# Performance work log

Hardware: AMD Instinct MI355X
Metric: run time of the kernel (lower is better)

## Reference

```python
import jax, jax.numpy as jnp
import numpy as np

B, T, D = 4, 2048, 1024
H = 16
HD = D // H  # 64


def setup_inputs() -> dict:
    key = jax.random.key(0)
    ks = jax.random.split(key, 7)
    scale = 1.0 / np.sqrt(D)
    x = jax.random.normal(ks[0], (B, T, D), dtype=jnp.float32)
    # per-head projection weights, stacked over heads: [H, D, HD]
    Wq = jax.random.normal(ks[1], (H, D, HD), dtype=jnp.float32) * scale
    Wk = jax.random.normal(ks[2], (H, D, HD), dtype=jnp.float32) * scale
    Wv = jax.random.normal(ks[3], (H, D, HD), dtype=jnp.float32) * scale
    s_raw = jnp.zeros((H,), dtype=jnp.float32)  # learnable ssmax scale per head
    proj_W = jax.random.normal(ks[4], (D, D), dtype=jnp.float32) * scale
    proj_b = jax.random.normal(ks[5], (D,), dtype=jnp.float32) * 0.01
    return {"x": x, "Wq": Wq, "Wk": Wk, "Wv": Wv, "s_raw": s_raw,
            "proj_W": proj_W, "proj_b": proj_b}


def reference(x, Wq, Wk, Wv, s_raw, proj_W, proj_b):
    # per-head q/k/v: [B, H, T, HD]
    q = jnp.einsum('btd,hde->bhte', x, Wq)
    k = jnp.einsum('btd,hde->bhte', x, Wk)
    v = jnp.einsum('btd,hde->bhte', x, Wv)

    # ssmax: q scaled by softplus(s) * log(position index, 1-based)
    logn = jnp.log(jnp.arange(1, T + 1, dtype=x.dtype))  # [T]
    s = jax.nn.softplus(s_raw)  # [H]
    q = q * (s[None, :, None, None] * logn[None, None, :, None])

    scores = jnp.einsum('bhte,bhse->bhts', q, k) * (HD ** -0.5)
    causal = jnp.tril(jnp.ones((T, T), dtype=bool))
    scores = jnp.where(causal[None, None], scores, -jnp.inf)
    w = jax.nn.softmax(scores, axis=-1)

    out = jnp.einsum('bhts,bhse->bhte', w, v)          # [B, H, T, HD]
    out = out.transpose(0, 2, 1, 3).reshape(B, T, D)    # concat heads
    return out @ proj_W.T + proj_b
```

## Files before the change

### kernel.cpp

```cpp
#include <hip/hip_runtime.h>
#include <hip/hip_bf16.h>

#define Bv 4
#define Tv 2048
#define Dv 1024
#define Hv 16
#define HDv 64
#define Mv (Bv*Tv)

typedef __hip_bfloat16 bf16;
typedef short s8v __attribute__((ext_vector_type(8)));
typedef float f4v __attribute__((ext_vector_type(4)));
typedef float f16a __attribute__((ext_vector_type(16)));

__device__ __forceinline__ unsigned short f2us(float x){
    bf16 h = __float2bfloat16(x);
    return *reinterpret_cast<unsigned short*>(&h);
}
__device__ __forceinline__ unsigned int pack2(float a, float b){
    return (unsigned int)f2us(a) | ((unsigned int)f2us(b) << 16);
}
__device__ __forceinline__ void glds16(const unsigned short* g, unsigned short* lds_base){
    __builtin_amdgcn_global_load_lds(
        (const __attribute__((address_space(1))) unsigned int*)g,
        (__attribute__((address_space(3))) unsigned int*)lds_base, 16, 0, 0);
}

__global__ void cvt_kernel(const float* __restrict__ src,
                           unsigned short* __restrict__ dst, int n4) {
    int i = blockIdx.x * 256 + threadIdx.x;
    if (i < n4) {
        float4 f = *(const float4*)(src + (size_t)i * 4);
        ushort4 o;
        o.x = f2us(f.x); o.y = f2us(f.y); o.z = f2us(f.z); o.w = f2us(f.w);
        *(ushort4*)(dst + (size_t)i * 4) = o;
    }
}

__global__ __launch_bounds__(256) void wt_kernel(
    const float* __restrict__ Wq, const float* __restrict__ Wk,
    const float* __restrict__ Wv, unsigned short* __restrict__ Wt)
{
    const int dt  = blockIdx.x;
    const int h   = blockIdx.y;
    const int sel = blockIdx.z;
    const float* W = (sel == 0) ? Wq : ((sel == 1) ? Wk : Wv);
    const float* Wh = W + (size_t)h * Dv * HDv;
    __shared__ float Tf[64][65];
    const int tid = threadIdx.x;
    for (int l = 0; l < 16; ++l) {
        int idx = tid + l * 256;
        int r = idx >> 6, e = idx & 63;
        Tf[r][e] = Wh[(size_t)(dt * 64 + r) * HDv + e];
    }
    __syncthreads();
    unsigned short* out = Wt + ((size_t)sel * Hv + h) * HDv * Dv;
    for (int l = 0; l < 16; ++l) {
        int idx = tid + l * 256;
        int e = idx >> 6, d = idx & 63;
        out[(size_t)e * Dv + dt * 64 + d] = f2us(Tf[d][e]);
    }
}

__global__ __launch_bounds__(256) void qkv_big(
    const unsigned short* __restrict__ xb, const unsigned short* __restrict__ Wc,
    const float* __restrict__ s_raw,
    unsigned short* __restrict__ q, unsigned short* __restrict__ k,
    unsigned short* __restrict__ vT)
{
    const int bm = blockIdx.x;
    const int bn = blockIdx.y;
    const int tid = threadIdx.x;
    const int w = tid >> 6, lane = tid & 63;
    const int n16 = lane & 15, quad = lane >> 4;
    const int wm = w >> 1, wn = w & 1;

    __shared__ __align__(16) unsigned short As[128 * 64];
    __shared__ __align__(16) unsigned short Bs[128 * 64];

    f4v acc[4][4];
    f4v zero = {0.f, 0.f, 0.f, 0.f};
    #pragma unroll
    for (int i = 0; i < 4; ++i)
        #pragma unroll
        for (int j = 0; j < 4; ++j) acc[i][j] = zero;

    const int row0 = bm * 128, col0 = bn * 128;
    const int lr = lane >> 3, lc = (lane & 7) * 8;

    for (int k0 = 0; k0 < Dv; k0 += 64) {
        __syncthreads();
        #pragma unroll
        for (int i = 0; i < 4; ++i) {
            int rb = w * 32 + i * 8;
            glds16(xb + (size_t)(row0 + rb + lr) * Dv + k0 + lc, &As[rb * 64]);
            glds16(Wc + (size_t)(col0 + rb + lr) * Dv + k0 + lc, &Bs[rb * 64]);
        }
        __syncthreads();
        #pragma unroll
        for (int ks = 0; ks < 2; ++ks) {
            s8v bfr[4];
            #pragma unroll
            for (int ni = 0; ni < 4; ++ni)
                bfr[ni] = *(const s8v*)(&Bs[(wn * 64 + ni * 16 + n16) * 64 + ks * 32 + quad * 8]);
            #pragma unroll
            for (int mi = 0; mi < 4; ++mi) {
                s8v afr = *(const s8v*)(&As[(wm * 64 + mi * 16 + n16) * 64 + ks * 32 + quad * 8]);
                #pragma unroll
                for (int ni = 0; ni < 4; ++ni)
                    acc[mi][ni] = __builtin_amdgcn_mfma_f32_16x16x32_bf16(afr, bfr[ni], acc[mi][ni], 0, 0, 0);
            }
        }
    }

    #pragma unroll
    for (int ni = 0; ni < 4; ++ni) {
        int n = col0 + wn * 64 + ni * 16 + n16;
        int sel = n >> 10, h = (n >> 6) & 15, e = n & 63;
        if (sel == 2) {
            #pragma unroll
            for (int mi = 0; mi < 4; ++mi) {
                int row = row0 + wm * 64 + mi * 16 + quad * 4;
                int bb_ = row >> 11, t = row & (Tv - 1);
                ushort4 o4;
                o4.x = f2us(acc[mi][ni][0]); o4.y = f2us(acc[mi][ni][1]);
                o4.z = f2us(acc[mi][ni][2]); o4.w = f2us(acc[mi][ni][3]);
                *(ushort4*)(vT + ((size_t)(bb_ * Hv + h) * HDv + e) * Tv + t) = o4;
            }
        } else {
            unsigned short* out = (sel == 0) ? q : k;
            float sc_h = (sel == 0) ? log1pf(expf(s_raw[h])) * 0.125f : 1.0f;
            #pragma unroll
            for (int mi = 0; mi < 4; ++mi) {
                #pragma unroll
                for (int r = 0; r < 4; ++r) {
                    int row = row0 + wm * 64 + mi * 16 + quad * 4 + r;
                    int bb_ = row >> 11, t = row & (Tv - 1);
                    float rs = (sel == 0) ? sc_h * logf((float)(t + 1)) : 1.0f;
                    out[((size_t)(bb_ * Hv + h) * Tv + t) * HDv + e] = f2us(acc[mi][ni][r] * rs);
                }
            }
        }
    }
}

__global__ __launch_bounds__(256) void attn_mfma(
    const unsigned short* __restrict__ q, const unsigned short* __restrict__ k,
    const unsigned short* __restrict__ vT, unsigned short* __restrict__ attn)
{
    const int qt = (Tv / 128 - 1) - (int)blockIdx.x;
    const int bh = blockIdx.y;
    const int b = bh >> 4, h = bh & 15;
    const int tid = threadIdx.x;
    const int w = tid >> 6, lane = tid & 63;
    const int l31 = lane & 31, hi = lane >> 5;

    __shared__ __align__(16) unsigned short Ks[64][72];
    __shared__ __align__(16) unsigned short VTs[64][72];

    const size_t hb = (size_t)(b * Hv + h) * Tv * HDv;
    const int qstrip = qt * 128 + w * 32;
    const int myq = qstrip + l31;

    s8v qf[4];
    #pragma unroll
    for (int ks = 0; ks < 4; ++ks)
        qf[ks] = *(const s8v*)(q + hb + (size_t)myq * HDv + ks * 16 + hi * 8);

    f16a st0, st1, ot0, ot1;
    #pragma unroll
    for (int i = 0; i < 16; ++i) { ot0[i] = 0.f; ot1[i] = 0.f; }
    float lrun = 0.f;

    const int r_ = tid >> 3, g_ = (tid & 7) * 8;
    const int r2 = (tid + 256) >> 3, g2 = (tid & 7) * 8;

    ulonglong2 kr0, kr1, vr0, vr1;
    kr0 = *(const ulonglong2*)(k + hb + (size_t)r_ * HDv + g_);
    vr0 = *(const ulonglong2*)(vT + hb + (size_t)r_ * Tv + 0 + g_);
    kr1 = *(const ulonglong2*)(k + hb + (size_t)r2 * HDv + g2);
    vr1 = *(const ulonglong2*)(vT + hb + (size_t)r2 * Tv + 0 + g2);

    const int ktmax = 2 * qt + 1;
    for (int kt = 0; kt <= ktmax; ++kt) {
        const int s0 = kt * 64;
        __syncthreads();
        *(ulonglong2*)(&Ks[r_][g_]) = kr0;
        *(ulonglong2*)(&VTs[r_][g_]) = vr0;
        *(ulonglong2*)(&Ks[r2][g2]) = kr1;
        *(ulonglong2*)(&VTs[r2][g2]) = vr1;
        __syncthreads();
        if (kt < ktmax) {
            const int sn = s0 + 64;
            kr0 = *(const ulonglong2*)(k + hb + (size_t)(sn + r_) * HDv + g_);
            vr0 = *(const ulonglong2*)(vT + hb + (size_t)r_ * Tv + sn + g_);
            kr1 = *(const ulonglong2*)(k + hb + (size_t)(sn + r2) * HDv + g2);
            vr1 = *(const ulonglong2*)(vT + hb + (size_t)r2 * Tv + sn + g2);
        }
        if (s0 > qstrip + 31) continue;

        #pragma unroll
        for (int i = 0; i < 16; ++i) { st0[i] = 0.f; st1[i] = 0.f; }
        #pragma unroll
        for (int ks = 0; ks < 4; ++ks) {
            s8v a0 = *(const s8v*)(&Ks[l31][ks * 16 + hi * 8]);
            s8v a1 = *(const s8v*)(&Ks[32 + l31][ks * 16 + hi * 8]);
            st0 = __builtin_amdgcn_mfma_f32_32x32x16_bf16(a0, qf[ks], st0, 0, 0, 0);
            st1 = __builtin_amdgcn_mfma_f32_32x32x16_bf16(a1, qf[ks], st1, 0, 0, 0);
        }
        if (s0 + 63 > qstrip) {
            #pragma unroll
            for (int reg = 0; reg < 16; ++reg) {
                int srow = (reg & 3) + 8 * (reg >> 2) + 4 * hi;
                if (s0 + srow > myq)      st0[reg] = -1e30f;
                if (s0 + 32 + srow > myq) st1[reg] = -1e30f;
            }
        }
        float lsum = 0.f;
        #pragma unroll
        for (int i = 0; i < 16; ++i) {
            st0[i] = __expf(st0[i]);
            st1[i] = __expf(st1[i]);
            lsum += st0[i] + st1[i];
        }
        lrun += lsum;

        unsigned int pk[16];
        #pragma unroll
        for (int g = 0; g < 4; ++g) {
            pk[2 * g]         = pack2(st0[4 * g],     st0[4 * g + 1]);
            pk[2 * g + 1]     = pack2(st0[4 * g + 2], st0[4 * g + 3]);
            pk[8 + 2 * g]     = pack2(st1[4 * g],     st1[4 * g + 1]);
            pk[8 + 2 * g + 1] = pack2(st1[4 * g + 2], st1[4 * g + 3]);
        }
        #pragma unroll
        for (int ks = 0; ks < 4; ++ks) {
            int base = (ks >> 1) * 8 + (ks & 1) * 4;
            unsigned int v0 = hi ? pk[base]     : pk[base + 2];
            unsigned int v1 = hi ? pk[base + 1] : pk[base + 3];
            unsigned int r0 = (unsigned int)__shfl_xor((int)v0, 32);
            unsigned int r1 = (unsigned int)__shfl_xor((int)v1, 32);
            union { s8v v; unsigned int d[4]; } bf;
            bf.d[0] = hi ? r0 : pk[base];
            bf.d[1] = hi ? r1 : pk[base + 1];
            bf.d[2] = hi ? pk[base + 2] : r0;
            bf.d[3] = hi ? pk[base + 3] : r1;
            s8v a0 = *(const s8v*)(&VTs[l31][ks * 16 + hi * 8]);
            s8v a1 = *(const s8v*)(&VTs[32 + l31][ks * 16 + hi * 8]);
            ot0 = __builtin_amdgcn_mfma_f32_32x32x16_bf16(a0, bf.v, ot0, 0, 0, 0);
            ot1 = __builtin_amdgcn_mfma_f32_32x32x16_bf16(a1, bf.v, ot1, 0, 0, 0);
        }
    }

    float ltot = lrun + __shfl_xor(lrun, 32);
    float inv = 1.0f / ltot;
    size_t obase = ((size_t)(b * Tv) + myq) * Dv + h * HDv;
    #pragma unroll
    for (int g = 0; g < 4; ++g) {
        ushort4 o4;
        o4.x = f2us(ot0[4 * g]     * inv); o4.y = f2us(ot0[4 * g + 1] * inv);
        o4.z = f2us(ot0[4 * g + 2] * inv); o4.w = f2us(ot0[4 * g + 3] * inv);
        *(ushort4*)(attn + obase + 8 * g + 4 * hi) = o4;
        o4.x = f2us(ot1[4 * g]     * inv); o4.y = f2us(ot1[4 * g + 1] * inv);
        o4.z = f2us(ot1[4 * g + 2] * inv); o4.w = f2us(ot1[4 * g + 3] * inv);
        *(ushort4*)(attn + obase + 32 + 8 * g + 4 * hi) = o4;
    }
}

__global__ __launch_bounds__(256) void proj_big(
    const unsigned short* __restrict__ attn, const unsigned short* __restrict__ Wb,
    const float* __restrict__ bias, float* __restrict__ out)
{
    const int bm = blockIdx.x;
    const int bn = blockIdx.y;
    const int tid = threadIdx.x;
    const int w = tid >> 6, lane = tid & 63;
    const int n16 = lane & 15, quad = lane >> 4;
    const int wm = w >> 1, wn = w & 1;

    __shared__ __align__(16) unsigned short As[128 * 64];
    __shared__ __align__(16) unsigned short Bs[128 * 64];

    f4v acc[4][4];
    f4v zero = {0.f, 0.f, 0.f, 0.f};
    #pragma unroll
    for (int i = 0; i < 4; ++i)
        #pragma unroll
        for (int j = 0; j < 4; ++j) acc[i][j] = zero;

    const int row0 = bm * 128, col0 = bn * 128;
    const int lr = lane >> 3, lc = (lane & 7) * 8;

    for (int k0 = 0; k0 < Dv; k0 += 64) {
        __syncthreads();
        #pragma unroll
        for (int i = 0; i < 4; ++i) {
            int rb = w * 32 + i * 8;
            glds16(attn + (size_t)(row0 + rb + lr) * Dv + k0 + lc, &As[rb * 64]);
            glds16(Wb   + (size_t)(col0 + rb + lr) * Dv + k0 + lc, &Bs[rb * 64]);
        }
        __syncthreads();
        #pragma unroll
        for (int ks = 0; ks < 2; ++ks) {
            s8v bfr[4];
            #pragma unroll
            for (int ni = 0; ni < 4; ++ni)
                bfr[ni] = *(const s8v*)(&Bs[(wn * 64 + ni * 16 + n16) * 64 + ks * 32 + quad * 8]);
            #pragma unroll
            for (int mi = 0; mi < 4; ++mi) {
                s8v afr = *(const s8v*)(&As[(wm * 64 + mi * 16 + n16) * 64 + ks * 32 + quad * 8]);
                #pragma unroll
                for (int ni = 0; ni < 4; ++ni)
                    acc[mi][ni] = __builtin_amdgcn_mfma_f32_16x16x32_bf16(afr, bfr[ni], acc[mi][ni], 0, 0, 0);
            }
        }
    }
    #pragma unroll
    for (int ni = 0; ni < 4; ++ni) {
        int n = col0 + wn * 64 + ni * 16 + n16;
        float bn_ = bias[n];
        #pragma unroll
        for (int mi = 0; mi < 4; ++mi) {
            #pragma unroll
            for (int r = 0; r < 4; ++r) {
                int m = row0 + wm * 64 + mi * 16 + quad * 4 + r;
                out[(size_t)m * Dv + n] = acc[mi][ni][r] + bn_;
            }
        }
    }
}

extern "C" void kernel_launch(void* const* d_in, const int* in_sizes, int n_in,
                              void* d_out, int out_size, void* d_ws, size_t ws_size,
                              hipStream_t stream) {
    const float* x     = (const float*)d_in[0];
    const float* Wq    = (const float*)d_in[1];
    const float* Wk    = (const float*)d_in[2];
    const float* Wv    = (const float*)d_in[3];
    const float* s_raw = (const float*)d_in[4];
    const float* projW = (const float*)d_in[5];
    const float* projb = (const float*)d_in[6];
    float* out = (float*)d_out;

    const size_t nx  = (size_t)Mv * Dv;
    const size_t nqk = (size_t)Bv * Hv * Tv * HDv;
    unsigned short* x_bf = (unsigned short*)d_ws;
    unsigned short* qb   = x_bf + nx;
    unsigned short* kb   = qb + nqk;
    unsigned short* vTb  = kb + nqk;
    unsigned short* Wt   = vTb + nqk;
    unsigned short* Wpb  = Wt + (size_t)3 * Hv * HDv * Dv;
    unsigned short* attn = x_bf;

    cvt_kernel<<<(int)(nx / 4 / 256), 256, 0, stream>>>(x, x_bf, (int)(nx / 4));
    cvt_kernel<<<(int)((size_t)Dv * Dv / 4 / 256), 256, 0, stream>>>(projW, Wpb, Dv * Dv / 4);
    wt_kernel<<<dim3(16, 16, 3), 256, 0, stream>>>(Wq, Wk, Wv, Wt);
    qkv_big<<<dim3(Mv / 128, 3072 / 128), 256, 0, stream>>>(x_bf, Wt, s_raw, qb, kb, vTb);
    attn_mfma<<<dim3(Tv / 128, Bv * Hv), 256, 0, stream>>>(qb, kb, vTb, attn);
    proj_big<<<dim3(Mv / 128, Dv / 128), 256, 0, stream>>>(attn, Wpb, projb, out);
}
```

Baseline: 326.5 us.

## Load K/V MFMA operands directly from global memory, dropping LDS staging

The attention kernel no longer stages K and V^T tiles through shared memory with block-wide barriers and register prefetch. Each wave now loads its MFMA operand fragments straight from global memory and runs only up to its own causal limit, with no __syncthreads. This removes barrier and LDS traffic and lets each wave stop at its own diagonal, but the four waves of a block now each fetch the same K/V data through cache and lose the software prefetch, so load latency is exposed.

```diff
diff --git a/kernel.cpp b/kernel.cpp
--- a/kernel.cpp
+++ b/kernel.cpp
@@ -155,10 +155,9 @@
     const int w = tid >> 6, lane = tid & 63;
     const int l31 = lane & 31, hi = lane >> 5;
 
-    __shared__ __align__(16) unsigned short Ks[64][72];
-    __shared__ __align__(16) unsigned short VTs[64][72];
-
     const size_t hb = (size_t)(b * Hv + h) * Tv * HDv;
+    const unsigned short* kb = k + hb;
+    const unsigned short* vb = vT + hb;
     const int qstrip = qt * 128 + w * 32;
     const int myq = qstrip + l31;
 
@@ -172,41 +171,29 @@
     for (int i = 0; i < 16; ++i) { ot0[i] = 0.f; ot1[i] = 0.f; }
     float lrun = 0.f;
 
-    const int r_ = tid >> 3, g_ = (tid & 7) * 8;
-    const int r2 = (tid + 256) >> 3, g2 = (tid & 7) * 8;
-
-    ulonglong2 kr0, kr1, vr0, vr1;
-    kr0 = *(const ulonglong2*)(k + hb + (size_t)r_ * HDv + g_);
-    vr0 = *(const ulonglong2*)(vT + hb + (size_t)r_ * Tv + 0 + g_);
-    kr1 = *(const ulonglong2*)(k + hb + (size_t)r2 * HDv + g2);
-    vr1 = *(const ulonglong2*)(vT + hb + (size_t)r2 * Tv + 0 + g2);
-
-    const int ktmax = 2 * qt + 1;
+    const int ktmax = (qstrip + 31) >> 6;
     for (int kt = 0; kt <= ktmax; ++kt) {
         const int s0 = kt * 64;
-        __syncthreads();
-        *(ulonglong2*)(&Ks[r_][g_]) = kr0;
-        *(ulonglong2*)(&VTs[r_][g_]) = vr0;
-        *(ulonglong2*)(&Ks[r2][g2]) = kr1;
-        *(ulonglong2*)(&VTs[r2][g2]) = vr1;
-        __syncthreads();
-        if (kt < ktmax) {
-            const int sn = s0 + 64;
-            kr0 = *(const ulonglong2*)(k + hb + (size_t)(sn + r_) * HDv + g_);
-            vr0 = *(const ulonglong2*)(vT + hb + (size_t)r_ * Tv + sn + g_);
-            kr1 = *(const ulonglong2*)(k + hb + (size_t)(sn + r2) * HDv + g2);
-            vr1 = *(const ulonglong2*)(vT + hb + (size_t)r2 * Tv + sn + g2);
-        }
-        if (s0 > qstrip + 31) continue;
+
+        s8v ka0[4], ka1[4];
+        #pragma unroll
+        for (int ks = 0; ks < 4; ++ks) {
+            ka0[ks] = *(const s8v*)(kb + (size_t)(s0 + l31) * HDv + ks * 16 + hi * 8);
+            ka1[ks] = *(const s8v*)(kb + (size_t)(s0 + 32 + l31) * HDv + ks * 16 + hi * 8);
+        }
+        s8v va0[4], va1[4];
+        #pragma unroll
+        for (int ks = 0; ks < 4; ++ks) {
+            va0[ks] = *(const s8v*)(vb + (size_t)l31 * Tv + s0 + ks * 16 + hi * 8);
+            va1[ks] = *(const s8v*)(vb + (size_t)(32 + l31) * Tv + s0 + ks * 16 + hi * 8);
+        }
 
         #pragma unroll
         for (int i = 0; i < 16; ++i) { st0[i] = 0.f; st1[i] = 0.f; }
         #pragma unroll
         for (int ks = 0; ks < 4; ++ks) {
-            s8v a0 = *(const s8v*)(&Ks[l31][ks * 16 + hi * 8]);
-            s8v a1 = *(const s8v*)(&Ks[32 + l31][ks * 16 + hi * 8]);
-            st0 = __builtin_amdgcn_mfma_f32_32x32x16_bf16(a0, qf[ks], st0, 0, 0, 0);
-            st1 = __builtin_amdgcn_mfma_f32_32x32x16_bf16(a1, qf[ks], st1, 0, 0, 0);
+            st0 = __builtin_amdgcn_mfma_f32_32x32x16_bf16(ka0[ks], qf[ks], st0, 0, 0, 0);
+            st1 = __builtin_amdgcn_mfma_f32_32x32x16_bf16(ka1[ks], qf[ks], st1, 0, 0, 0);
         }
         if (s0 + 63 > qstrip) {
             #pragma unroll
@@ -245,10 +232,8 @@
             bf.d[1] = hi ? r1 : pk[base + 1];
             bf.d[2] = hi ? pk[base + 2] : r0;
             bf.d[3] = hi ? pk[base + 3] : r1;
-            s8v a0 = *(const s8v*)(&VTs[l31][ks * 16 + hi * 8]);
-            s8v a1 = *(const s8v*)(&VTs[32 + l31][ks * 16 + hi * 8]);
-            ot0 = __builtin_amdgcn_mfma_f32_32x32x16_bf16(a0, bf.v, ot0, 0, 0, 0);
-            ot1 = __builtin_amdgcn_mfma_f32_32x32x16_bf16(a1, bf.v, ot1, 0, 0, 0);
+            ot0 = __builtin_amdgcn_mfma_f32_32x32x16_bf16(va0[ks], bf.v, ot0, 0, 0, 0);
+            ot1 = __builtin_amdgcn_mfma_f32_32x32x16_bf16(va1[ks], bf.v, ot1, 0, 0, 0);
         }
     }
 
```

Result: slower. 443.4 us (+35.8%).
